# Kernel optimization log

Measured on AMD Instinct MI355X. Metric: run time of the kernel, lower is better.

## Reference

```python
import jax, jax.numpy as jnp
import numpy as np

BZ, D_IN, D_STATE, D_OUT, L = 8, 256, 512, 256, 4096


def setup_inputs() -> dict:
    key = jax.random.key(0)
    k_u, k_a, k_b, k_c = jax.random.split(key, 4)
    init_scale = 0.5
    u = jax.random.normal(k_u, (BZ, D_IN, L), dtype=jnp.float32)
    A_unconstrained = jax.random.normal(k_a, (D_STATE,), dtype=jnp.float32) * 0.1
    B_mat = jax.random.normal(k_b, (D_STATE, D_IN), dtype=jnp.float32) * init_scale / np.sqrt(D_IN)
    C_mat = jax.random.normal(k_c, (D_OUT, D_STATE), dtype=jnp.float32) * init_scale / np.sqrt(D_STATE)
    D_mat = jnp.zeros((D_OUT, D_IN), dtype=jnp.float32)
    h0 = jnp.zeros((D_STATE,), dtype=jnp.float32)
    return {"u": u, "A_unconstrained": A_unconstrained, "B_mat": B_mat,
            "C_mat": C_mat, "D_mat": D_mat, "h0": h0}


def reference(u, A_unconstrained, B_mat, C_mat, D_mat, h0):
    # u: (B, input_dim, L)
    Bz = u.shape[0]
    A_diag = -jax.nn.softplus(A_unconstrained)          # (S,)
    # Precompute input projection for all timesteps: (L, B, S)
    Bu = jnp.einsum('bil,si->lbs', u, B_mat)
    state0 = jnp.broadcast_to(h0[None, :], (Bz, A_diag.shape[0]))

    def step(state, bu_t):
        x_t = state * A_diag[None, :] + bu_t            # (B, S)
        return x_t, x_t

    _, xs = jax.lax.scan(step, state0, Bu)              # xs: (L, B, S)
    # y_t = x_t @ C^T + u_t @ D^T, assembled as (B, output_dim, L)
    Y = jnp.einsum('lbs,os->bol', xs, C_mat) + jnp.einsum('bil,oi->bol', u, D_mat)
    return Y
```

## Files before the change

kernel.cpp:

```cpp
#include <hip/hip_runtime.h>
#include <math.h>

#define BZ 8
#define DI 256
#define DS 512
#define DOUT 256
#define LL 4096
#define BS (BZ * DS)
#define CH 64
#define CT 64
#define TST 136

typedef __bf16 bf16x8 __attribute__((ext_vector_type(8)));
typedef float f32x4 __attribute__((ext_vector_type(4)));
typedef unsigned short us8 __attribute__((ext_vector_type(8)));

__device__ __forceinline__ ushort f2b(float f) {
    union { float f; unsigned u; } v; v.f = f;
    unsigned r = v.u + 0x7FFFu + ((v.u >> 16) & 1u);
    return (ushort)(r >> 16);
}
__device__ __forceinline__ float b2f(ushort h) {
    union { unsigned u; float f; } v; v.u = ((unsigned)h) << 16;
    return v.f;
}

__device__ __forceinline__ void gload16(const ushort* g, ushort* l) {
    __builtin_amdgcn_global_load_lds(
        (const __attribute__((address_space(1))) unsigned int*)g,
        (__attribute__((address_space(3))) unsigned int*)l,
        16, 0, 0);
}

__global__ __launch_bounds__(256) void k_prep_u2t(const float* __restrict__ u,
                                                  ushort* __restrict__ utr,
                                                  const float* __restrict__ Au,
                                                  float* __restrict__ apow,
                                                  const float* __restrict__ Bm,
                                                  const float* __restrict__ Cm,
                                                  const float* __restrict__ Dm,
                                                  ushort* __restrict__ Bmb,
                                                  ushort* __restrict__ Cmb,
                                                  ushort* __restrict__ Dmb,
                                                  int* __restrict__ dflag) {
    __shared__ float T[64][65];
    const int tid = threadIdx.x;
    const int id = blockIdx.x;
    if (id < 2048) {
        const int l0 = (id & 63) * 64;
        const int i0 = ((id >> 6) & 3) * 64;
        const int b  = id >> 8;
        const int r = tid >> 4, c4 = tid & 15;
#pragma unroll
        for (int rr = r; rr < 64; rr += 16) {
            float4 v = *(const float4*)&u[((size_t)b * DI + i0 + rr) * LL + l0 + c4 * 4];
            T[rr][c4 * 4 + 0] = v.x; T[rr][c4 * 4 + 1] = v.y;
            T[rr][c4 * 4 + 2] = v.z; T[rr][c4 * 4 + 3] = v.w;
        }
        __syncthreads();
#pragma unroll
        for (int ll = r; ll < 64; ll += 16) {
            ushort4 o;
            o.x = f2b(T[c4 * 4 + 0][ll]); o.y = f2b(T[c4 * 4 + 1][ll]);
            o.z = f2b(T[c4 * 4 + 2][ll]); o.w = f2b(T[c4 * 4 + 3][ll]);
            *(ushort4*)&utr[((size_t)b * LL + l0 + ll) * DI + i0 + c4 * 4] = o;
        }
    } else {
        const int t = (id - 2048) * 256 + tid;
        const int n1 = DS * DI / 4, n2 = DOUT * DS / 4, n3 = DOUT * DI / 4;
        if (t < n1) {
            float4 v = ((const float4*)Bm)[t];
            ushort4 o; o.x = f2b(v.x); o.y = f2b(v.y); o.z = f2b(v.z); o.w = f2b(v.w);
            ((ushort4*)Bmb)[t] = o;
        } else if (t < n1 + n2) {
            float4 v = ((const float4*)Cm)[t - n1];
            ushort4 o; o.x = f2b(v.x); o.y = f2b(v.y); o.z = f2b(v.z); o.w = f2b(v.w);
            ((ushort4*)Cmb)[t - n1] = o;
        } else if (t < n1 + n2 + n3) {
            float4 v = ((const float4*)Dm)[t - n1 - n2];
            ushort4 o; o.x = f2b(v.x); o.y = f2b(v.y); o.z = f2b(v.z); o.w = f2b(v.w);
            ((ushort4*)Dmb)[t - n1 - n2] = o;
            if (v.x != 0.f || v.y != 0.f || v.z != 0.f || v.w != 0.f)
                atomicOr(dflag, 1);
        }
        if (t < DS) {
            float x = Au[t];
            float sp = (x > 15.f) ? x : log1pf(expf(x));
            float ad = -sp;
            float p = 1.f;
            apow[t] = 1.f;
            for (int j = 1; j <= CT; ++j) { p *= ad; apow[j * DS + t] = p; }
        }
    }
}

__global__ __launch_bounds__(256) void k_bu(const ushort* __restrict__ Bmb,
                                            const ushort* __restrict__ utr,
                                            ushort* __restrict__ Xb,
                                            float* __restrict__ finals,
                                            const float* __restrict__ apow) {
    __shared__ ushort smem[128 * TST];
    const int tid = threadIdx.x;
    const int w = tid >> 6, lane = tid & 63;
    const int l0 = blockIdx.x * 128, s0 = blockIdx.y * 128, b = blockIdx.z;
    const int wm = w & 1, wn = w >> 1;
    const int mrow = lane & 15, quad = lane >> 4;
    const int sr = lane >> 2, sc = (lane & 3) * 8;
    const int off0 = (16 * w) * 32, off1 = (16 * w + 64) * 32;

    f32x4 acc[4][4];
#pragma unroll
    for (int mi = 0; mi < 4; ++mi)
#pragma unroll
        for (int ni = 0; ni < 4; ++ni) acc[mi][ni] = (f32x4)0.f;

    const ushort* ag0 = Bmb + (size_t)(s0 + 16 * w + sr) * DI + sc;
    const ushort* ag1 = ag0 + (size_t)64 * DI;
    const ushort* bg0 = utr + ((size_t)b * LL + l0 + 16 * w + sr) * DI + sc;
    const ushort* bg1 = bg0 + (size_t)64 * DI;

    gload16(ag0, smem + off0); gload16(ag1, smem + off1);
    gload16(bg0, smem + 8192 + off0); gload16(bg1, smem + 8192 + off1);

    for (int it = 0; it < DI / 32; ++it) {
        __syncthreads();
        const int cb = (it & 1) * 4096, nb = 4096 - cb;
        if (it + 1 < DI / 32) {
            const int kk = (it + 1) * 32;
            gload16(ag0 + kk, smem + nb + off0); gload16(ag1 + kk, smem + nb + off1);
            gload16(bg0 + kk, smem + 8192 + nb + off0); gload16(bg1 + kk, smem + 8192 + nb + off1);
        }
        bf16x8 af[4], bfr[4];
#pragma unroll
        for (int mi = 0; mi < 4; ++mi)
            af[mi] = *(const bf16x8*)&smem[cb + (wm * 64 + mi * 16 + mrow) * 32 + quad * 8];
#pragma unroll
        for (int ni = 0; ni < 4; ++ni)
            bfr[ni] = *(const bf16x8*)&smem[8192 + cb + (wn * 64 + ni * 16 + mrow) * 32 + quad * 8];
#pragma unroll
        for (int mi = 0; mi < 4; ++mi)
#pragma unroll
            for (int ni = 0; ni < 4; ++ni)
                acc[mi][ni] = __builtin_amdgcn_mfma_f32_16x16x32_bf16(af[mi], bfr[ni], acc[mi][ni], 0, 0, 0);
    }
    __syncthreads();

#pragma unroll
    for (int mi = 0; mi < 4; ++mi) {
        const int sloc = wm * 64 + mi * 16 + quad * 4;
#pragma unroll
        for (int ni = 0; ni < 4; ++ni) {
            const int lloc = wn * 64 + ni * 16 + mrow;
            f32x4 v = acc[mi][ni];
            ushort4 o; o.x = f2b(v[0]); o.y = f2b(v[1]); o.z = f2b(v[2]); o.w = f2b(v[3]);
            *(ushort4*)&smem[lloc * TST + sloc] = o;
        }
    }
    __syncthreads();
    {
        const int cloc = tid >> 7, sl = tid & 127;
        const float a = apow[DS + s0 + sl];
        float acc2 = 0.f;
        ushort* p = &smem[(cloc * 64) * TST + sl];
#pragma unroll 8
        for (int j = 0; j < CT; ++j) {
            acc2 = a * acc2 + b2f(*p);
            *p = f2b(acc2);
            p += TST;
        }
        finals[(size_t)(l0 / 64 + cloc) * BS + (size_t)b * DS + s0 + sl] = acc2;
    }
    __syncthreads();
    {
        const int rr = tid >> 4, cc = tid & 15;
#pragma unroll
        for (int rep = 0; rep < 8; ++rep) {
            const int l = rep * 16 + rr;
            us8 v = *(const us8*)&smem[l * TST + cc * 8];
            *(us8*)&Xb[(size_t)(l0 + l) * BS + (size_t)b * DS + s0 + cc * 8] = v;
        }
    }
}

__global__ __launch_bounds__(256) void k_carry(const float* __restrict__ finals,
                                               float* __restrict__ carries,
                                               const float* __restrict__ apow,
                                               const float* __restrict__ h0) {
    const int bs = blockIdx.x * 256 + threadIdx.x;
    const int s = bs & (DS - 1);
    const float aT = apow[CT * DS + s];
    float carry = h0[s];
#pragma unroll 8
    for (int c = 0; c < CH; ++c) {
        carries[(size_t)c * BS + bs] = carry;
        carry = aT * carry + finals[(size_t)c * BS + bs];
    }
}

__global__ __launch_bounds__(256) void k_out(const ushort* __restrict__ Cmb,
                                             const ushort* __restrict__ Dmb,
                                             const ushort* __restrict__ Xb,
                                             const ushort* __restrict__ utr,
                                             const float* __restrict__ carries,
                                             const float* __restrict__ apow,
                                             const int* __restrict__ dflag,
                                             float* __restrict__ Y) {
    __shared__ ushort smem[13312];
    const int tid = threadIdx.x;
    const int w = tid >> 6, lane = tid & 63;
    const int l0 = blockIdx.x * 64, o0 = blockIdx.y * 128, b = blockIdx.z;
    const int mrow = lane & 15, quad = lane >> 4;
    const int sr = lane >> 2, sc = (lane & 3) * 8;
    const int off0 = (16 * w) * 32, off1 = (16 * w + 64) * 32;
    const int dnz = *dflag;

    f32x4 acc[4][2];
#pragma unroll
    for (int mi = 0; mi < 4; ++mi)
#pragma unroll
        for (int ni = 0; ni < 2; ++ni) acc[mi][ni] = (f32x4)0.f;

    auto compute = [&](const int aoff, const int ast, const int boff) {
        bf16x8 af[4], bfr[2];
#pragma unroll
        for (int mi = 0; mi < 4; ++mi)
            af[mi] = *(const bf16x8*)&smem[aoff + (mi * 16 + mrow) * ast + quad * 8];
#pragma unroll
        for (int ni = 0; ni < 2; ++ni)
            bfr[ni] = *(const bf16x8*)&smem[boff + (32 * w + ni * 16 + mrow) * 32 + quad * 8];
#pragma unroll
        for (int mi = 0; mi < 4; ++mi)
#pragma unroll
            for (int ni = 0; ni < 2; ++ni)
                acc[mi][ni] = __builtin_amdgcn_mfma_f32_16x16x32_bf16(af[mi], bfr[ni], acc[mi][ni], 0, 0, 0);
    };

    {
        const int r0 = 16 * w + sr;
        const int c0 = l0 >> 6;
        const float* ap0 = &apow[(size_t)(r0 + 1) * DS];
        const float* cr0 = &carries[(size_t)c0 * BS + (size_t)b * DS];
        const ushort* x0 = Xb + (size_t)(l0 + r0) * BS + (size_t)b * DS;
        const ushort* bg0 = Cmb + (size_t)(o0 + r0) * DS + sc;
        const ushort* bg1 = bg0 + (size_t)64 * DS;

        us8 xr; float4 par, pbr, car, cbr;
        auto loadX = [&](int it) {
            const int col = it * 32 + sc;
            xr  = *(const us8*)&x0[col];
            par = *(const float4*)&ap0[col];  pbr = *(const float4*)&ap0[col + 4];
            car = *(const float4*)&cr0[col];  cbr = *(const float4*)&cr0[col + 4];
        };
        auto storeA = [&](int dstoff) {
            us8 o;
            o[0] = f2b(b2f(xr[0]) + par.x * car.x); o[1] = f2b(b2f(xr[1]) + par.y * car.y);
            o[2] = f2b(b2f(xr[2]) + par.z * car.z); o[3] = f2b(b2f(xr[3]) + par.w * car.w);
            o[4] = f2b(b2f(xr[4]) + pbr.x * cbr.x); o[5] = f2b(b2f(xr[5]) + pbr.y * cbr.y);
            o[6] = f2b(b2f(xr[6]) + pbr.z * cbr.z); o[7] = f2b(b2f(xr[7]) + pbr.w * cbr.w);
            *(us8*)&smem[dstoff + r0 * 40 + sc] = o;
        };

        loadX(0); storeA(0);
        gload16(bg0, smem + 5120 + off0); gload16(bg1, smem + 5120 + off1);

        for (int it = 0; it < DS / 32; ++it) {
            __syncthreads();
            const int ca_ = (it & 1) * 2560, na_ = 2560 - ca_;
            const int cb_ = 5120 + (it & 1) * 4096, nb_ = 5120 + 4096 - (it & 1) * 4096;
            const bool more = (it + 1 < DS / 32);
            if (more) {
                const int kk = (it + 1) * 32;
                gload16(bg0 + kk, smem + nb_ + off0); gload16(bg1 + kk, smem + nb_ + off1);
                loadX(it + 1);
            }
            compute(ca_, 40, cb_);
            if (more) storeA(na_);
        }
    }
    if (dnz) {
        const ushort* ag0 = utr + ((size_t)b * LL + l0 + 16 * w + sr) * DI + sc;
        const ushort* bg0 = Dmb + (size_t)(o0 + 16 * w + sr) * DI + sc;
        const ushort* bg1 = bg0 + (size_t)64 * DI;

        __syncthreads();
        gload16(ag0, smem + off0);
        gload16(bg0, smem + 5120 + off0); gload16(bg1, smem + 5120 + off1);

        for (int it = 0; it < DI / 32; ++it) {
            __syncthreads();
            const int ca_ = (it & 1) * 2560, na_ = 2560 - ca_;
            const int cb_ = 5120 + (it & 1) * 4096, nb_ = 5120 + 4096 - (it & 1) * 4096;
            if (it + 1 < DI / 32) {
                const int kk = (it + 1) * 32;
                gload16(ag0 + kk, smem + na_ + off0);
                gload16(bg0 + kk, smem + nb_ + off0); gload16(bg1 + kk, smem + nb_ + off1);
            }
            compute(ca_, 32, cb_);
        }
    }

#pragma unroll
    for (int mi = 0; mi < 4; ++mi) {
        const int l = l0 + mi * 16 + quad * 4;
#pragma unroll
        for (int ni = 0; ni < 2; ++ni) {
            const int o = o0 + 32 * w + ni * 16 + mrow;
            *(float4*)&Y[((size_t)b * DOUT + o) * LL + l] = *(float4*)&acc[mi][ni];
        }
    }
}

extern "C" void kernel_launch(void* const* d_in, const int* in_sizes, int n_in,
                              void* d_out, int out_size, void* d_ws, size_t ws_size,
                              hipStream_t stream) {
    const float* u  = (const float*)d_in[0];
    const float* Au = (const float*)d_in[1];
    const float* Bm = (const float*)d_in[2];
    const float* Cm = (const float*)d_in[3];
    const float* Dm = (const float*)d_in[4];
    const float* h0 = (const float*)d_in[5];
    float* Y = (float*)d_out;

    char* p = (char*)d_ws;
    ushort* utr    = (ushort*)p; p += (size_t)BZ * LL * DI * 2;
    ushort* Xb     = (ushort*)p; p += (size_t)LL * BS * 2;
    float* finals  = (float*)p;  p += (size_t)CH * BS * 4;
    float* carries = (float*)p;  p += (size_t)CH * BS * 4;
    float* apow    = (float*)p;  p += (size_t)(CT + 1) * DS * 4;
    ushort* Bmb    = (ushort*)p; p += (size_t)DS * DI * 2;
    ushort* Cmb    = (ushort*)p; p += (size_t)DOUT * DS * 2;
    ushort* Dmb    = (ushort*)p; p += (size_t)DOUT * DI * 2;
    int* dflag     = (int*)p;    p += 16;

    hipMemsetAsync(dflag, 0, 4, stream);
    k_prep_u2t<<<dim3(2368), 256, 0, stream>>>(u, utr, Au, apow, Bm, Cm, Dm, Bmb, Cmb, Dmb, dflag);
    k_bu<<<dim3(LL / 128, DS / 128, BZ), 256, 0, stream>>>(Bmb, utr, Xb, finals, apow);
    k_carry<<<dim3(BS / 256), 256, 0, stream>>>(finals, carries, apow, h0);
    k_out<<<dim3(LL / 64, DOUT / 128, BZ), 256, 0, stream>>>(Cmb, Dmb, Xb, utr, carries, apow, dflag, Y);
}
```

Before: 144.0 us.

## Fuse carry scan into output kernel and deepen GEMM prefetch pipelines

Removes the separate k_carry launch. Each k_out block now recomputes its chunk carry by scanning the chunk finals up to its own chunk index and keeps the result in LDS. Both k_bu and k_out switch from __syncthreads double buffering to a triple-buffered B/C tile pipeline that waits with explicit vmcnt/lgkmcnt counts and raw s_barrier. In exchange, blocks with later chunk indices do more redundant serial carry work, up to 63 steps over global finals.

Result: slower. 150.7 us (+4.6%).

```diff
diff --git a/kernel.cpp b/kernel.cpp
--- a/kernel.cpp
+++ b/kernel.cpp
@@ -14,6 +14,9 @@
 typedef __bf16 bf16x8 __attribute__((ext_vector_type(8)));
 typedef float f32x4 __attribute__((ext_vector_type(4)));
 typedef unsigned short us8 __attribute__((ext_vector_type(8)));
+
+#define WAITV(n) asm volatile("s_waitcnt vmcnt(" #n ")" ::: "memory")
+#define WAITL0   asm volatile("s_waitcnt lgkmcnt(0)" ::: "memory")
 
 __device__ __forceinline__ ushort f2b(float f) {
     union { float f; unsigned u; } v; v.f = f;
@@ -99,7 +102,7 @@
                                             ushort* __restrict__ Xb,
                                             float* __restrict__ finals,
                                             const float* __restrict__ apow) {
-    __shared__ ushort smem[128 * TST];
+    __shared__ ushort smem[20480];
     const int tid = threadIdx.x;
     const int w = tid >> 6, lane = tid & 63;
     const int l0 = blockIdx.x * 128, s0 = blockIdx.y * 128, b = blockIdx.z;
@@ -119,24 +122,30 @@
     const ushort* bg0 = utr + ((size_t)b * LL + l0 + 16 * w + sr) * DI + sc;
     const ushort* bg1 = bg0 + (size_t)64 * DI;
 
-    gload16(ag0, smem + off0); gload16(ag1, smem + off1);
-    gload16(bg0, smem + 8192 + off0); gload16(bg1, smem + 8192 + off1);
-
+    gload16(ag0, smem + off0);                 gload16(ag1, smem + off1);
+    gload16(bg0, smem + 8192 + off0);          gload16(bg1, smem + 8192 + off1);
+    gload16(bg0 + 32, smem + 12288 + off0);    gload16(bg1 + 32, smem + 12288 + off1);
+
+#pragma unroll
     for (int it = 0; it < DI / 32; ++it) {
-        __syncthreads();
-        const int cb = (it & 1) * 4096, nb = 4096 - cb;
+        if (it < 7) { WAITV(2); } else { WAITV(0); }
+        __builtin_amdgcn_s_barrier();
         if (it + 1 < DI / 32) {
-            const int kk = (it + 1) * 32;
-            gload16(ag0 + kk, smem + nb + off0); gload16(ag1 + kk, smem + nb + off1);
-            gload16(bg0 + kk, smem + 8192 + nb + off0); gload16(bg1 + kk, smem + 8192 + nb + off1);
-        }
+            const int kk = (it + 1) * 32, ab = ((it + 1) & 1) * 4096;
+            gload16(ag0 + kk, smem + ab + off0); gload16(ag1 + kk, smem + ab + off1);
+        }
+        if (it + 2 < DI / 32) {
+            const int kk = (it + 2) * 32, bb = 8192 + ((it + 2) % 3) * 4096;
+            gload16(bg0 + kk, smem + bb + off0); gload16(bg1 + kk, smem + bb + off1);
+        }
+        const int ca = (it & 1) * 4096, cb = 8192 + (it % 3) * 4096;
         bf16x8 af[4], bfr[4];
 #pragma unroll
         for (int mi = 0; mi < 4; ++mi)
-            af[mi] = *(const bf16x8*)&smem[cb + (wm * 64 + mi * 16 + mrow) * 32 + quad * 8];
+            af[mi] = *(const bf16x8*)&smem[ca + (wm * 64 + mi * 16 + mrow) * 32 + quad * 8];
 #pragma unroll
         for (int ni = 0; ni < 4; ++ni)
-            bfr[ni] = *(const bf16x8*)&smem[8192 + cb + (wn * 64 + ni * 16 + mrow) * 32 + quad * 8];
+            bfr[ni] = *(const bf16x8*)&smem[cb + (wn * 64 + ni * 16 + mrow) * 32 + quad * 8];
 #pragma unroll
         for (int mi = 0; mi < 4; ++mi)
 #pragma unroll
@@ -182,30 +191,17 @@
     }
 }
 
-__global__ __launch_bounds__(256) void k_carry(const float* __restrict__ finals,
-                                               float* __restrict__ carries,
-                                               const float* __restrict__ apow,
-                                               const float* __restrict__ h0) {
-    const int bs = blockIdx.x * 256 + threadIdx.x;
-    const int s = bs & (DS - 1);
-    const float aT = apow[CT * DS + s];
-    float carry = h0[s];
-#pragma unroll 8
-    for (int c = 0; c < CH; ++c) {
-        carries[(size_t)c * BS + bs] = carry;
-        carry = aT * carry + finals[(size_t)c * BS + bs];
-    }
-}
-
 __global__ __launch_bounds__(256) void k_out(const ushort* __restrict__ Cmb,
                                              const ushort* __restrict__ Dmb,
                                              const ushort* __restrict__ Xb,
                                              const ushort* __restrict__ utr,
-                                             const float* __restrict__ carries,
+                                             const float* __restrict__ finals,
                                              const float* __restrict__ apow,
+                                             const float* __restrict__ h0,
                                              const int* __restrict__ dflag,
                                              float* __restrict__ Y) {
-    __shared__ ushort smem[13312];
+    __shared__ ushort smem[18432];
+    float* crl = (float*)&smem[17408];
     const int tid = threadIdx.x;
     const int w = tid >> 6, lane = tid & 63;
     const int l0 = blockIdx.x * 64, o0 = blockIdx.y * 128, b = blockIdx.z;
@@ -214,6 +210,20 @@
     const int off0 = (16 * w) * 32, off1 = (16 * w + 64) * 32;
     const int dnz = *dflag;
 
+    {
+        const int c0 = blockIdx.x;
+        const float aT0 = apow[CT * DS + tid];
+        const float aT1 = apow[CT * DS + 256 + tid];
+        float cva = h0[tid], cvb = h0[256 + tid];
+        const float* fb = finals + (size_t)b * DS;
+        for (int c = 0; c < c0; ++c) {
+            cva = aT0 * cva + fb[(size_t)c * BS + tid];
+            cvb = aT1 * cvb + fb[(size_t)c * BS + 256 + tid];
+        }
+        crl[tid] = cva; crl[256 + tid] = cvb;
+    }
+    __syncthreads();
+
     f32x4 acc[4][2];
 #pragma unroll
     for (int mi = 0; mi < 4; ++mi)
@@ -237,44 +247,58 @@
 
     {
         const int r0 = 16 * w + sr;
-        const int c0 = l0 >> 6;
         const float* ap0 = &apow[(size_t)(r0 + 1) * DS];
-        const float* cr0 = &carries[(size_t)c0 * BS + (size_t)b * DS];
         const ushort* x0 = Xb + (size_t)(l0 + r0) * BS + (size_t)b * DS;
         const ushort* bg0 = Cmb + (size_t)(o0 + r0) * DS + sc;
         const ushort* bg1 = bg0 + (size_t)64 * DS;
 
-        us8 xr; float4 par, pbr, car, cbr;
+        us8 xr[2]; float4 par[2], pbr[2];
         auto loadX = [&](int it) {
+            const int sl = it & 1;
             const int col = it * 32 + sc;
-            xr  = *(const us8*)&x0[col];
-            par = *(const float4*)&ap0[col];  pbr = *(const float4*)&ap0[col + 4];
-            car = *(const float4*)&cr0[col];  cbr = *(const float4*)&cr0[col + 4];
+            xr[sl]  = *(const us8*)&x0[col];
+            par[sl] = *(const float4*)&ap0[col];
+            pbr[sl] = *(const float4*)&ap0[col + 4];
         };
-        auto storeA = [&](int dstoff) {
+        auto storeA = [&](int it, int dstoff) {
+            const int sl = it & 1;
+            const int col = it * 32 + sc;
+            float4 c_a = *(const float4*)&crl[col];
+            float4 c_b = *(const float4*)&crl[col + 4];
             us8 o;
-            o[0] = f2b(b2f(xr[0]) + par.x * car.x); o[1] = f2b(b2f(xr[1]) + par.y * car.y);
-            o[2] = f2b(b2f(xr[2]) + par.z * car.z); o[3] = f2b(b2f(xr[3]) + par.w * car.w);
-            o[4] = f2b(b2f(xr[4]) + pbr.x * cbr.x); o[5] = f2b(b2f(xr[5]) + pbr.y * cbr.y);
-            o[6] = f2b(b2f(xr[6]) + pbr.z * cbr.z); o[7] = f2b(b2f(xr[7]) + pbr.w * cbr.w);
+            o[0] = f2b(b2f(xr[sl][0]) + par[sl].x * c_a.x);
+            o[1] = f2b(b2f(xr[sl][1]) + par[sl].y * c_a.y);
+            o[2] = f2b(b2f(xr[sl][2]) + par[sl].z * c_a.z);
+            o[3] = f2b(b2f(xr[sl][3]) + par[sl].w * c_a.w);
+            o[4] = f2b(b2f(xr[sl][4]) + pbr[sl].x * c_b.x);
+            o[5] = f2b(b2f(xr[sl][5]) + pbr[sl].y * c_b.y);
+            o[6] = f2b(b2f(xr[sl][6]) + pbr[sl].z * c_b.z);
+            o[7] = f2b(b2f(xr[sl][7]) + pbr[sl].w * c_b.w);
             *(us8*)&smem[dstoff + r0 * 40 + sc] = o;
         };
 
-        loadX(0); storeA(0);
-        gload16(bg0, smem + 5120 + off0); gload16(bg1, smem + 5120 + off1);
-
+        loadX(0);
+        gload16(bg0, smem + 5120 + off0);      gload16(bg1, smem + 5120 + off1);
+        gload16(bg0 + 32, smem + 9216 + off0); gload16(bg1 + 32, smem + 9216 + off1);
+        loadX(1);
+        storeA(0, 0);
+        WAITL0;
+
+#pragma unroll
         for (int it = 0; it < DS / 32; ++it) {
-            __syncthreads();
-            const int ca_ = (it & 1) * 2560, na_ = 2560 - ca_;
-            const int cb_ = 5120 + (it & 1) * 4096, nb_ = 5120 + 4096 - (it & 1) * 4096;
-            const bool more = (it + 1 < DS / 32);
-            if (more) {
-                const int kk = (it + 1) * 32;
-                gload16(bg0 + kk, smem + nb_ + off0); gload16(bg1 + kk, smem + nb_ + off1);
-                loadX(it + 1);
+            if (it < 15) { WAITV(5); } else { WAITV(0); }
+            __builtin_amdgcn_s_barrier();
+            if (it + 2 < DS / 32) {
+                loadX(it + 2);
+                const int kk = (it + 2) * 32, bb = 5120 + ((it + 2) % 3) * 4096;
+                gload16(bg0 + kk, smem + bb + off0);
+                gload16(bg1 + kk, smem + bb + off1);
             }
-            compute(ca_, 40, cb_);
-            if (more) storeA(na_);
+            compute((it & 1) * 2560, 40, 5120 + (it % 3) * 4096);
+            if (it + 1 < DS / 32) {
+                storeA(it + 1, ((it + 1) & 1) * 2560);
+                WAITL0;
+            }
         }
     }
     if (dnz) {
@@ -325,7 +349,6 @@
     ushort* utr    = (ushort*)p; p += (size_t)BZ * LL * DI * 2;
     ushort* Xb     = (ushort*)p; p += (size_t)LL * BS * 2;
     float* finals  = (float*)p;  p += (size_t)CH * BS * 4;
-    float* carries = (float*)p;  p += (size_t)CH * BS * 4;
     float* apow    = (float*)p;  p += (size_t)(CT + 1) * DS * 4;
     ushort* Bmb    = (ushort*)p; p += (size_t)DS * DI * 2;
     ushort* Cmb    = (ushort*)p; p += (size_t)DOUT * DS * 2;
@@ -335,6 +358,5 @@
     hipMemsetAsync(dflag, 0, 4, stream);
     k_prep_u2t<<<dim3(2368), 256, 0, stream>>>(u, utr, Au, apow, Bm, Cm, Dm, Bmb, Cmb, Dmb, dflag);
     k_bu<<<dim3(LL / 128, DS / 128, BZ), 256, 0, stream>>>(Bmb, utr, Xb, finals, apow);
-    k_carry<<<dim3(BS / 256), 256, 0, stream>>>(finals, carries, apow, h0);
-    k_out<<<dim3(LL / 64, DOUT / 128, BZ), 256, 0, stream>>>(Cmb, Dmb, Xb, utr, carries, apow, dflag, Y);
-}
+    k_out<<<dim3(LL / 64, DOUT / 128, BZ), 256, 0, stream>>>(Cmb, Dmb, Xb, utr, finals, apow, h0, dflag, Y);
+}
```
